# Kernel optimization log

Measured on AMD Instinct MI355X. Metric: run time of the kernel, lower is better.

## Reference

```python
import jax, jax.numpy as jnp
import numpy as np

B, T, H, NUM_LAYERS = 256, 1024, 128, 2


def _lstm_layer(x, W_ih, W_hh, b_ih, b_hh):
    """Single LSTM layer, PyTorch gate order (i, f, g, o).
    x: [B, T, in], W_ih: [4H, in], W_hh: [4H, H], biases: [4H]. Returns [B, T, H].
    """
    Bv = x.shape[0]
    Hv = W_hh.shape[1]
    # Precompute input-to-gate projections for all timesteps (big GEMM outside scan)
    xg = jnp.einsum('bti,gi->btg', x, W_ih) + b_ih + b_hh  # [B, T, 4H]

    def step(carry, xg_t):
        h, c = carry
        g = xg_t + h @ W_hh.T  # [B, 4H]
        i, f, gg, o = jnp.split(g, 4, axis=-1)
        i = jax.nn.sigmoid(i)
        f = jax.nn.sigmoid(f)
        gg = jnp.tanh(gg)
        o = jax.nn.sigmoid(o)
        c = f * c + i * gg
        h = o * jnp.tanh(c)
        return (h, c), h

    h0 = jnp.zeros((Bv, Hv), x.dtype)
    c0 = jnp.zeros((Bv, Hv), x.dtype)
    _, hs = jax.lax.scan(step, (h0, c0), jnp.swapaxes(xg, 0, 1))  # hs: [T, B, H]
    return jnp.swapaxes(hs, 0, 1)


def setup_inputs() -> dict:
    key = jax.random.key(0)
    ks = jax.random.split(key, 11)
    s = 1.0 / np.sqrt(H)  # PyTorch LSTM init scale
    inp = {
        'x': jax.random.normal(ks[0], (B, T, 1), dtype=jnp.float32),
        'W_ih0': jax.random.uniform(ks[1], (4 * H, 1), minval=-s, maxval=s, dtype=jnp.float32),
        'W_hh0': jax.random.uniform(ks[2], (4 * H, H), minval=-s, maxval=s, dtype=jnp.float32),
        'b_ih0': jax.random.uniform(ks[3], (4 * H,), minval=-s, maxval=s, dtype=jnp.float32),
        'b_hh0': jax.random.uniform(ks[4], (4 * H,), minval=-s, maxval=s, dtype=jnp.float32),
        'W_ih1': jax.random.uniform(ks[5], (4 * H, H), minval=-s, maxval=s, dtype=jnp.float32),
        'W_hh1': jax.random.uniform(ks[6], (4 * H, H), minval=-s, maxval=s, dtype=jnp.float32),
        'b_ih1': jax.random.uniform(ks[7], (4 * H,), minval=-s, maxval=s, dtype=jnp.float32),
        'b_hh1': jax.random.uniform(ks[8], (4 * H,), minval=-s, maxval=s, dtype=jnp.float32),
        'fc_w': jax.random.uniform(ks[9], (1, H), minval=-s, maxval=s, dtype=jnp.float32),
        'fc_b': jax.random.uniform(ks[10], (1,), minval=-s, maxval=s, dtype=jnp.float32),
    }
    return inp


def reference(x, W_ih0, W_hh0, b_ih0, b_hh0, W_ih1, W_hh1, b_ih1, b_hh1, fc_w, fc_b):
    h = _lstm_layer(x, W_ih0, W_hh0, b_ih0, b_hh0)   # [B, T, H]
    h = _lstm_layer(h, W_ih1, W_hh1, b_ih1, b_hh1)   # [B, T, H]
    out = jnp.einsum('bth,oh->bto', h, fc_w) + fc_b  # [B, T, 1]
    return out
```

## Files before the change

kernel.cpp:

```cpp
#include <hip/hip_runtime.h>

#define TT 1024
#define HH 128

typedef unsigned int u32;
typedef unsigned short u16;
typedef _Float16 f16;
typedef f16 f16x2 __attribute__((ext_vector_type(2)));
typedef f16 f16x8 __attribute__((ext_vector_type(8)));
typedef float f32x4 __attribute__((ext_vector_type(4)));
typedef u32 u32x4 __attribute__((ext_vector_type(4)));

#define MFMA16(A, B, C) __builtin_amdgcn_mfma_f32_16x16x32_f16((A), (B), (C), 0, 0, 0)
#define K2L2E 2.8853900817779268f

__device__ __forceinline__ float ex2(float x) {
#if __has_builtin(__builtin_amdgcn_exp2f)
    return __builtin_amdgcn_exp2f(x);
#else
    extern "C" __device__ float __ocml_exp2_f32(float);
    return __ocml_exp2_f32(x);
#endif
}
__device__ __forceinline__ float rcp_(float x) { return __builtin_amdgcn_rcpf(x); }

__device__ __forceinline__ float fdot2_(u32 w, u32 h, float acc) {
#if __has_builtin(__builtin_amdgcn_fdot2)
    return __builtin_amdgcn_fdot2(__builtin_bit_cast(f16x2, w),
                                  __builtin_bit_cast(f16x2, h), acc, false);
#else
    const f16x2 a = __builtin_bit_cast(f16x2, w);
    const f16x2 b = __builtin_bit_cast(f16x2, h);
    return fmaf((float)a.y, (float)b.y, fmaf((float)a.x, (float)b.x, acc));
#endif
}

__device__ __forceinline__ float dpp_mov(float v, const int ctrl) {
    int t;
    switch (ctrl) {
      case 0x00: t = __builtin_amdgcn_update_dpp(0, __float_as_int(v), 0x00, 0xF, 0xF, true); break;
      case 0x55: t = __builtin_amdgcn_update_dpp(0, __float_as_int(v), 0x55, 0xF, 0xF, true); break;
      case 0xAA: t = __builtin_amdgcn_update_dpp(0, __float_as_int(v), 0xAA, 0xF, 0xF, true); break;
      case 0xFF: t = __builtin_amdgcn_update_dpp(0, __float_as_int(v), 0xFF, 0xF, 0xF, true); break;
      case 0xB1: t = __builtin_amdgcn_update_dpp(0, __float_as_int(v), 0xB1, 0xF, 0xF, true); break;
      default:   t = __builtin_amdgcn_update_dpp(0, __float_as_int(v), 0x4E, 0xF, 0xF, true); break;
    }
    return __int_as_float(t);
}
__device__ __forceinline__ float dpp_add(float v, const int ctrl) {
    int t;
    switch (ctrl) {
      case 0xB1:  t = __builtin_amdgcn_update_dpp(0, __float_as_int(v), 0xB1,  0xF, 0xF, true); break;
      case 0x4E:  t = __builtin_amdgcn_update_dpp(0, __float_as_int(v), 0x4E,  0xF, 0xF, true); break;
      case 0x141: t = __builtin_amdgcn_update_dpp(0, __float_as_int(v), 0x141, 0xF, 0xF, true); break;
      default:    t = __builtin_amdgcn_update_dpp(0, __float_as_int(v), 0x140, 0xF, 0xF, true); break;
    }
    return v + __int_as_float(t);
}

__device__ __forceinline__ int hswz(int iu) {
    return (iu & 0x30) + (((((iu >> 2) & 3) + (iu >> 4)) & 3) << 2) + (iu & 3);
}

__device__ __forceinline__ float xpose4(float a0, float a1, float a2, float a3, int q) {
    const bool qb0 = (q & 1) != 0;
    float s0, s1;
    {
        const float send = qb0 ? a0 : a1;
        s0 = (qb0 ? a1 : a0) + dpp_mov(send, 0xB1);
    }
    {
        const float send = qb0 ? a2 : a3;
        s1 = (qb0 ? a3 : a2) + dpp_mov(send, 0xB1);
    }
    const bool qb1 = (q & 2) != 0;
    const float send = qb1 ? s0 : s1;
    return (qb1 ? s1 : s0) + dpp_mov(send, 0x4E);
}

__global__ void prep(const float* __restrict__ Whh0, const float* __restrict__ Whh1,
                     const float* __restrict__ Wih1, const float* __restrict__ Wih0,
                     const float* __restrict__ bih0, const float* __restrict__ bhh0,
                     const float* __restrict__ bih1, const float* __restrict__ bhh1,
                     f16* __restrict__ Wpk0, f16* __restrict__ Wpk1,
                     f16* __restrict__ W1h,  f16* __restrict__ W1l,
                     float* __restrict__ bx0, float* __restrict__ wx0,
                     float* __restrict__ b1p)
{
    const int p = blockIdx.x;
    const int k = threadIdx.x;
    const int c = p & 3, u = p >> 2;
    const int g = c * 128 + u;
    const float sc = (c == 2) ? K2L2E : -1.4426950408889634f;

    Wpk0[p * HH + k] = (f16)(Whh0[(size_t)g * HH + k] * sc);
    Wpk1[p * HH + k] = (f16)(Whh1[(size_t)g * HH + k] * sc);
    const float wf = Wih1[(size_t)g * HH + k] * sc;
    const f16 wh = (f16)wf;
    W1h[p * HH + k] = wh;
    W1l[p * HH + k] = (f16)(wf - (float)wh);
    if (k == 0) {
        bx0[p] = (bih0[g] + bhh0[g]) * sc;
        wx0[p] = Wih0[g] * sc;
        b1p[p] = (bih1[g] + bhh1[g]) * sc;
    }
}

__global__ __launch_bounds__(512, 2) void lstm0(
    const float* __restrict__ x, const f16* __restrict__ Wpk0,
    const float* __restrict__ bx0, const float* __restrict__ wx0,
    f16* __restrict__ h0g)
{
    const int b = blockIdx.x;
    const int tid = threadIdx.x;
    const int u = tid >> 2, q = tid & 3;
    const bool is_g = (q == 2);
    const float Ag = is_g ? -2.f : 1.f;
    const float Cg = is_g ?  1.f : 0.f;

    __shared__ __align__(16) float xS[TT];
    __shared__ __align__(16) u32 hS[2][64];
    __shared__ __align__(16) u16 hO[32][HH];

    xS[tid]       = x[(size_t)b * TT + tid];
    xS[tid + 512] = x[(size_t)b * TT + tid + 512];
    if (tid < 128) ((u32*)hS)[tid] = 0u;

    u32x4 Wq[4][4];
#pragma unroll
    for (int c = 0; c < 4; ++c) {
        const u32* wp = (const u32*)Wpk0 + (size_t)((tid & ~3) + c) * 64 + q * 16;
#pragma unroll
        for (int rb = 0; rb < 4; ++rb) Wq[c][rb] = *(const u32x4*)(wp + rb * 4);
    }
    const float biasx = bx0[tid];
    const float wxv   = wx0[tid];
    float c1 = 0.f;
    __syncthreads();

    f16* og = h0g + (size_t)b * TT * HH;

#pragma unroll 1
    for (int t = 0; t < TT; ++t) {
        const u32* hcur = hS[t & 1];
        float a0 = 0.f, a1 = 0.f, a2 = 0.f, a3 = 0.f;
#pragma unroll
        for (int rb = 0; rb < 4; ++rb) {
            const u32x4 hq = *(const u32x4*)(hcur + (q << 4) + (((rb + q) & 3) << 2));
            a0 = fdot2_(Wq[0][rb].x, hq.x, a0); a0 = fdot2_(Wq[0][rb].y, hq.y, a0);
            a0 = fdot2_(Wq[0][rb].z, hq.z, a0); a0 = fdot2_(Wq[0][rb].w, hq.w, a0);
            a1 = fdot2_(Wq[1][rb].x, hq.x, a1); a1 = fdot2_(Wq[1][rb].y, hq.y, a1);
            a1 = fdot2_(Wq[1][rb].z, hq.z, a1); a1 = fdot2_(Wq[1][rb].w, hq.w, a1);
            a2 = fdot2_(Wq[2][rb].x, hq.x, a2); a2 = fdot2_(Wq[2][rb].y, hq.y, a2);
            a2 = fdot2_(Wq[2][rb].z, hq.z, a2); a2 = fdot2_(Wq[2][rb].w, hq.w, a2);
            a3 = fdot2_(Wq[3][rb].x, hq.x, a3); a3 = fdot2_(Wq[3][rb].y, hq.y, a3);
            a3 = fdot2_(Wq[3][rb].z, hq.z, a3); a3 = fdot2_(Wq[3][rb].w, hq.w, a3);
        }
        const float V = xpose4(a0, a1, a2, a3, q);
        const float a = V + fmaf(xS[t], wxv, biasx);
        const float act = fmaf(Ag, rcp_(1.f + ex2(a)), Cg);
        const float gi = dpp_mov(act, 0x00);
        const float gf = dpp_mov(act, 0x55);
        const float gg = dpp_mov(act, 0xAA);
        const float go = dpp_mov(act, 0xFF);
        c1 = fmaf(gf, c1, gi * gg);
        const float h = go * fmaf(-2.f, rcp_(1.f + ex2(K2L2E * c1)), 1.f);
        if (q == 0) {
            const u16 hb = __builtin_bit_cast(u16, (f16)h);
            ((u16*)hS[(t + 1) & 1])[2 * hswz(u >> 1) + (u & 1)] = hb;
            hO[t & 31][u] = hb;
        }
        __syncthreads();
        if ((t & 31) == 31) {
            *(u32x4*)((u16*)og + (size_t)(t - 31) * HH + tid * 8) =
                *(const u32x4*)(&hO[0][0] + tid * 8);
            __syncthreads();
        }
    }
}

__global__ __launch_bounds__(512, 2) void lstm1(
    const f16* __restrict__ h0g, const f16* __restrict__ Wpk1,
    const f16* __restrict__ W1h, const f16* __restrict__ W1l,
    const float* __restrict__ b1p, const float* __restrict__ fcw,
    const float* __restrict__ fcb, float* __restrict__ out)
{
    const int b = blockIdx.x;
    const int tid = threadIdx.x;
    const int u = tid >> 2, q = tid & 3;
    const int wv = tid >> 6, lane = tid & 63;
    const int lr = lane & 15, lq = lane >> 4;
    const bool is_g = (q == 2);
    const float Ag = is_g ? -2.f : 1.f;
    const float Cg = is_g ?  1.f : 0.f;

    __shared__ __align__(16) float xgS[32 * 512];
    __shared__ __align__(16) u32 hS1[2][64];
    __shared__ __align__(16) float fcP[32][16];

    if (tid < 128) ((u32*)hS1)[tid] = 0u;
    const float fcu025 = fcw[u] * 0.25f;
    const float fcbv = fcb[0];
    float c1 = 0.f;
    __syncthreads();

    const f16* hb0 = h0g + (size_t)b * TT * HH;
    float* ob = out + (size_t)b * TT;

#pragma unroll 1
    for (int t0 = 0; t0 < TT; t0 += 32) {
        {
            f16x8 B0[4], B1[4];
#pragma unroll
            for (int ks = 0; ks < 4; ++ks) {
                B0[ks] = *(const f16x8*)(hb0 + (size_t)(t0 + lr) * HH + ks * 32 + lq * 8);
                B1[ks] = *(const f16x8*)(hb0 + (size_t)(t0 + 16 + lr) * HH + ks * 32 + lq * 8);
            }
#pragma unroll
            for (int gtl = 0; gtl < 4; ++gtl) {
                const int g16 = (wv * 4 + gtl) * 16;
                const float4 bi = *(const float4*)&b1p[g16 + lq * 4];
                f32x4 a0 = {bi.x, bi.y, bi.z, bi.w};
                f32x4 a1 = a0;
#pragma unroll
                for (int ks = 0; ks < 4; ++ks) {
                    const f16x8 Ah = *(const f16x8*)(W1h + (size_t)(g16 + lr) * HH + ks * 32 + lq * 8);
                    const f16x8 Al = *(const f16x8*)(W1l + (size_t)(g16 + lr) * HH + ks * 32 + lq * 8);
                    a0 = MFMA16(Ah, B0[ks], a0);
                    a0 = MFMA16(Al, B0[ks], a0);
                    a1 = MFMA16(Ah, B1[ks], a1);
                    a1 = MFMA16(Al, B1[ks], a1);
                }
                const int gb = g16 + lq * 4;
                *(f32x4*)&xgS[lr * 512 + (gb ^ ((lr & 7) << 2))] = a0;
                *(f32x4*)&xgS[(16 + lr) * 512 + (gb ^ ((lr & 7) << 2))] = a1;
            }
        }
        __syncthreads();

        u32x4 Wq[4][4];
        {
            const u32* wb = (const u32*)Wpk1;
            asm volatile("" : "+v"(wb));
#pragma unroll
            for (int c = 0; c < 4; ++c) {
                const u32* wp = wb + (size_t)((tid & ~3) + c) * 64 + q * 16;
#pragma unroll
                for (int rb = 0; rb < 4; ++rb) Wq[c][rb] = *(const u32x4*)(wp + rb * 4);
            }
        }

#pragma unroll 1
        for (int i = 0; i < 32; ++i) {
            const int t = t0 + i;
            const u32* hcur = hS1[t & 1];
            float a0 = 0.f, a1 = 0.f, a2 = 0.f, a3 = 0.f;
#pragma unroll
            for (int rb = 0; rb < 4; ++rb) {
                const u32x4 hq = *(const u32x4*)(hcur + (q << 4) + (((rb + q) & 3) << 2));
                a0 = fdot2_(Wq[0][rb].x, hq.x, a0); a0 = fdot2_(Wq[0][rb].y, hq.y, a0);
                a0 = fdot2_(Wq[0][rb].z, hq.z, a0); a0 = fdot2_(Wq[0][rb].w, hq.w, a0);
                a1 = fdot2_(Wq[1][rb].x, hq.x, a1); a1 = fdot2_(Wq[1][rb].y, hq.y, a1);
                a1 = fdot2_(Wq[1][rb].z, hq.z, a1); a1 = fdot2_(Wq[1][rb].w, hq.w, a1);
                a2 = fdot2_(Wq[2][rb].x, hq.x, a2); a2 = fdot2_(Wq[2][rb].y, hq.y, a2);
                a2 = fdot2_(Wq[2][rb].z, hq.z, a2); a2 = fdot2_(Wq[2][rb].w, hq.w, a2);
                a3 = fdot2_(Wq[3][rb].x, hq.x, a3); a3 = fdot2_(Wq[3][rb].y, hq.y, a3);
                a3 = fdot2_(Wq[3][rb].z, hq.z, a3); a3 = fdot2_(Wq[3][rb].w, hq.w, a3);
            }
            const float V = xpose4(a0, a1, a2, a3, q);
            const float a = V + xgS[i * 512 + (tid ^ ((i & 7) << 2))];
            const float act = fmaf(Ag, rcp_(1.f + ex2(a)), Cg);
            const float gi = dpp_mov(act, 0x00);
            const float gf = dpp_mov(act, 0x55);
            const float gg = dpp_mov(act, 0xAA);
            const float go = dpp_mov(act, 0xFF);
            c1 = fmaf(gf, c1, gi * gg);
            const float h = go * fmaf(-2.f, rcp_(1.f + ex2(K2L2E * c1)), 1.f);
            if (q == 0)
                ((u16*)hS1[(t + 1) & 1])[2 * hswz(u >> 1) + (u & 1)] =
                    __builtin_bit_cast(u16, (f16)h);

            float pf = h * fcu025;
            pf = dpp_add(pf, 0xB1);
            pf = dpp_add(pf, 0x4E);
            pf = dpp_add(pf, 0x141);
            pf = dpp_add(pf, 0x140);
            pf += __int_as_float(__builtin_amdgcn_ds_swizzle(__float_as_int(pf), 0x401F));
            if ((lane & 31) == 0) fcP[i][wv * 2 + (lane >> 5)] = pf;
            __syncthreads();
        }

        if (tid < 32) {
            float s = 0.f;
#pragma unroll
            for (int r = 0; r < 4; ++r) {
                const float4 v = *(const float4*)&fcP[tid][r * 4];
                s += (v.x + v.y) + (v.z + v.w);
            }
            ob[t0 + tid] = s + fcbv;
        }
    }
}

extern "C" void kernel_launch(void* const* d_in, const int* in_sizes, int n_in,
                              void* d_out, int out_size, void* d_ws, size_t ws_size,
                              hipStream_t stream)
{
    const float* x    = (const float*)d_in[0];
    const float* Wih0 = (const float*)d_in[1];
    const float* Whh0 = (const float*)d_in[2];
    const float* bih0 = (const float*)d_in[3];
    const float* bhh0 = (const float*)d_in[4];
    const float* Wih1 = (const float*)d_in[5];
    const float* Whh1 = (const float*)d_in[6];
    const float* bih1 = (const float*)d_in[7];
    const float* bhh1 = (const float*)d_in[8];
    const float* fcw  = (const float*)d_in[9];
    const float* fcb  = (const float*)d_in[10];
    float* out = (float*)d_out;

    f16* h0g  = (f16*)d_ws;
    f16* Wpk0 = h0g + (size_t)256 * TT * HH;
    f16* Wpk1 = Wpk0 + 512 * HH;
    f16* W1h  = Wpk1 + 512 * HH;
    f16* W1l  = W1h + 512 * HH;
    float* bx0 = (float*)(W1l + 512 * HH);
    float* wx0 = bx0 + 512;
    float* b1p = wx0 + 512;

    prep <<<512, 128, 0, stream>>>(Whh0, Whh1, Wih1, Wih0, bih0, bhh0, bih1, bhh1,
                                   Wpk0, Wpk1, W1h, W1l, bx0, wx0, b1p);
    lstm0<<<256, 512, 0, stream>>>(x, Wpk0, bx0, wx0, h0g);
    lstm1<<<256, 512, 0, stream>>>(h0g, Wpk1, W1h, W1l, b1p, fcw, fcb, out);
}
```

Baseline: 1.269 ms.

## Split layer-0 recurrent dot products across 8 lanes with 1024-thread blocks

Layer-0 LSTM now uses 1024 threads per batch row, with each gate row's 128-wide dot product split across 8 lanes instead of 4. Partial sums are combined with an extra ds_swizzle, and the hidden state uses a padded shared-memory layout to avoid bank conflicts. This halves per-thread fdot2 work and register use on the serial critical path, at the cost of a cross-lane reduction and more threads sharing each barrier. Layer 1 also hoists its xg shared-memory load ahead of the dot products so the load latency overlaps with them.

```diff
diff --git a/kernel.cpp b/kernel.cpp
--- a/kernel.cpp
+++ b/kernel.cpp
@@ -10,6 +10,7 @@
 typedef f16 f16x8 __attribute__((ext_vector_type(8)));
 typedef float f32x4 __attribute__((ext_vector_type(4)));
 typedef u32 u32x4 __attribute__((ext_vector_type(4)));
+typedef u32 u32x2 __attribute__((ext_vector_type(2)));
 
 #define MFMA16(A, B, C) __builtin_amdgcn_mfma_f32_16x16x32_f16((A), (B), (C), 0, 0, 0)
 #define K2L2E 2.8853900817779268f
@@ -106,35 +107,36 @@
     }
 }
 
-__global__ __launch_bounds__(512, 2) void lstm0(
+__global__ __launch_bounds__(1024, 4) void lstm0(
     const float* __restrict__ x, const f16* __restrict__ Wpk0,
     const float* __restrict__ bx0, const float* __restrict__ wx0,
     f16* __restrict__ h0g)
 {
     const int b = blockIdx.x;
     const int tid = threadIdx.x;
-    const int u = tid >> 2, q = tid & 3;
+    const int u = tid >> 3, s = tid & 7;
+    const int q = s & 3;
     const bool is_g = (q == 2);
     const float Ag = is_g ? -2.f : 1.f;
     const float Cg = is_g ?  1.f : 0.f;
 
     __shared__ __align__(16) float xS[TT];
-    __shared__ __align__(16) u32 hS[2][64];
+    __shared__ __align__(16) u32 hS[2][96];
     __shared__ __align__(16) u16 hO[32][HH];
 
-    xS[tid]       = x[(size_t)b * TT + tid];
-    xS[tid + 512] = x[(size_t)b * TT + tid + 512];
-    if (tid < 128) ((u32*)hS)[tid] = 0u;
-
-    u32x4 Wq[4][4];
+    xS[tid] = x[(size_t)b * TT + tid];
+    if (tid < 192) ((u32*)hS)[tid] = 0u;
+
+    u32x4 Wq[4][2];
 #pragma unroll
     for (int c = 0; c < 4; ++c) {
-        const u32* wp = (const u32*)Wpk0 + (size_t)((tid & ~3) + c) * 64 + q * 16;
-#pragma unroll
-        for (int rb = 0; rb < 4; ++rb) Wq[c][rb] = *(const u32x4*)(wp + rb * 4);
-    }
-    const float biasx = bx0[tid];
-    const float wxv   = wx0[tid];
+        const u32* wp = (const u32*)Wpk0 + (size_t)(4 * u + c) * 64 + s * 8;
+        Wq[c][0] = *(const u32x4*)wp;
+        Wq[c][1] = *(const u32x4*)(wp + 4);
+    }
+    const int p_lane = 4 * u + q;
+    const float biasx = bx0[p_lane];
+    const float wxv   = wx0[p_lane];
     float c1 = 0.f;
     __syncthreads();
 
@@ -142,11 +144,11 @@
 
 #pragma unroll 1
     for (int t = 0; t < TT; ++t) {
-        const u32* hcur = hS[t & 1];
+        const u32* hcur = hS[t & 1] + s * 12;
         float a0 = 0.f, a1 = 0.f, a2 = 0.f, a3 = 0.f;
 #pragma unroll
-        for (int rb = 0; rb < 4; ++rb) {
-            const u32x4 hq = *(const u32x4*)(hcur + (q << 4) + (((rb + q) & 3) << 2));
+        for (int rb = 0; rb < 2; ++rb) {
+            const u32x4 hq = *(const u32x4*)(hcur + rb * 4);
             a0 = fdot2_(Wq[0][rb].x, hq.x, a0); a0 = fdot2_(Wq[0][rb].y, hq.y, a0);
             a0 = fdot2_(Wq[0][rb].z, hq.z, a0); a0 = fdot2_(Wq[0][rb].w, hq.w, a0);
             a1 = fdot2_(Wq[1][rb].x, hq.x, a1); a1 = fdot2_(Wq[1][rb].y, hq.y, a1);
@@ -156,7 +158,8 @@
             a3 = fdot2_(Wq[3][rb].x, hq.x, a3); a3 = fdot2_(Wq[3][rb].y, hq.y, a3);
             a3 = fdot2_(Wq[3][rb].z, hq.z, a3); a3 = fdot2_(Wq[3][rb].w, hq.w, a3);
         }
-        const float V = xpose4(a0, a1, a2, a3, q);
+        float V = xpose4(a0, a1, a2, a3, q);
+        V += __int_as_float(__builtin_amdgcn_ds_swizzle(__float_as_int(V), 0x101F));
         const float a = V + fmaf(xS[t], wxv, biasx);
         const float act = fmaf(Ag, rcp_(1.f + ex2(a)), Cg);
         const float gi = dpp_mov(act, 0x00);
@@ -165,15 +168,15 @@
         const float go = dpp_mov(act, 0xFF);
         c1 = fmaf(gf, c1, gi * gg);
         const float h = go * fmaf(-2.f, rcp_(1.f + ex2(K2L2E * c1)), 1.f);
-        if (q == 0) {
+        if (s == 0) {
             const u16 hb = __builtin_bit_cast(u16, (f16)h);
-            ((u16*)hS[(t + 1) & 1])[2 * hswz(u >> 1) + (u & 1)] = hb;
+            ((u16*)hS[(t + 1) & 1])[2 * (12 * (u >> 4) + ((u >> 1) & 7)) + (u & 1)] = hb;
             hO[t & 31][u] = hb;
         }
         __syncthreads();
         if ((t & 31) == 31) {
-            *(u32x4*)((u16*)og + (size_t)(t - 31) * HH + tid * 8) =
-                *(const u32x4*)(&hO[0][0] + tid * 8);
+            *(u32x2*)((u16*)og + (size_t)(t - 31) * HH + tid * 4) =
+                *(const u32x2*)(&hO[0][0] + tid * 4);
             __syncthreads();
         }
     }
@@ -253,6 +256,7 @@
 #pragma unroll 1
         for (int i = 0; i < 32; ++i) {
             const int t = t0 + i;
+            const float xgv = xgS[i * 512 + (tid ^ ((i & 7) << 2))];
             const u32* hcur = hS1[t & 1];
             float a0 = 0.f, a1 = 0.f, a2 = 0.f, a3 = 0.f;
 #pragma unroll
@@ -268,7 +272,7 @@
                 a3 = fdot2_(Wq[3][rb].z, hq.z, a3); a3 = fdot2_(Wq[3][rb].w, hq.w, a3);
             }
             const float V = xpose4(a0, a1, a2, a3, q);
-            const float a = V + xgS[i * 512 + (tid ^ ((i & 7) << 2))];
+            const float a = V + xgv;
             const float act = fmaf(Ag, rcp_(1.f + ex2(a)), Cg);
             const float gi = dpp_mov(act, 0x00);
             const float gf = dpp_mov(act, 0x55);
@@ -330,6 +334,6 @@
 
     prep <<<512, 128, 0, stream>>>(Whh0, Whh1, Wih1, Wih0, bih0, bhh0, bih1, bhh1,
                                    Wpk0, Wpk1, W1h, W1l, bx0, wx0, b1p);
-    lstm0<<<256, 512, 0, stream>>>(x, Wpk0, bx0, wx0, h0g);
+    lstm0<<<256, 1024, 0, stream>>>(x, Wpk0, bx0, wx0, h0g);
     lstm1<<<256, 512, 0, stream>>>(h0g, Wpk1, W1h, W1l, b1p, fcw, fcb, out);
 }
```

After: 1.433 ms. 1.13x slower.

## Fuse both LSTM layers into one producer-consumer kernel with flag handoff

Applied to the files above, without the earlier changes.

Merges the layer-0 and layer-1 kernels into a single 512-block launch. The first 256 blocks run layer 0 and publish a per-batch progress flag after each 32-step chunk. The last 256 blocks spin on that flag and then run layer 1, so the two sequential recurrences overlap in time instead of running back to back. It depends on all 512 blocks being co-resident, since launch bounds rise to 4 blocks per CU; if they are not, the spin-wait can deadlock. It also adds a memset and flag polling overhead.

```diff
diff --git a/kernel.cpp b/kernel.cpp
--- a/kernel.cpp
+++ b/kernel.cpp
@@ -106,154 +106,50 @@
     }
 }
 
-__global__ __launch_bounds__(512, 2) void lstm0(
-    const float* __restrict__ x, const f16* __restrict__ Wpk0,
-    const float* __restrict__ bx0, const float* __restrict__ wx0,
-    f16* __restrict__ h0g)
+__global__ __launch_bounds__(512, 4) void lstm_pc(
+    const float* __restrict__ x,
+    const f16* __restrict__ Wpk0, const float* __restrict__ bx0,
+    const float* __restrict__ wx0, f16* __restrict__ h0g,
+    const f16* __restrict__ Wpk1, const f16* __restrict__ W1h,
+    const f16* __restrict__ W1l,  const float* __restrict__ b1p,
+    const float* __restrict__ fcw, const float* __restrict__ fcb,
+    float* __restrict__ out, int* __restrict__ flags)
 {
-    const int b = blockIdx.x;
     const int tid = threadIdx.x;
-    const int u = tid >> 2, q = tid & 3;
-    const bool is_g = (q == 2);
-    const float Ag = is_g ? -2.f : 1.f;
-    const float Cg = is_g ?  1.f : 0.f;
-
-    __shared__ __align__(16) float xS[TT];
-    __shared__ __align__(16) u32 hS[2][64];
-    __shared__ __align__(16) u16 hO[32][HH];
-
-    xS[tid]       = x[(size_t)b * TT + tid];
-    xS[tid + 512] = x[(size_t)b * TT + tid + 512];
-    if (tid < 128) ((u32*)hS)[tid] = 0u;
-
-    u32x4 Wq[4][4];
-#pragma unroll
-    for (int c = 0; c < 4; ++c) {
-        const u32* wp = (const u32*)Wpk0 + (size_t)((tid & ~3) + c) * 64 + q * 16;
-#pragma unroll
-        for (int rb = 0; rb < 4; ++rb) Wq[c][rb] = *(const u32x4*)(wp + rb * 4);
-    }
-    const float biasx = bx0[tid];
-    const float wxv   = wx0[tid];
-    float c1 = 0.f;
-    __syncthreads();
-
-    f16* og = h0g + (size_t)b * TT * HH;
+
+    __shared__ __align__(16) float bigS[32 * 512];
+    __shared__ __align__(16) u32 hSx[2][64];
+    __shared__ __align__(16) u16 hOx[32][HH];
+    __shared__ __align__(16) float fcPx[32][16];
+
+    if (blockIdx.x < 256) {
+        const int b = blockIdx.x;
+        const int u = tid >> 2, q = tid & 3;
+        const bool is_g = (q == 2);
+        const float Ag = is_g ? -2.f : 1.f;
+        const float Cg = is_g ?  1.f : 0.f;
+
+        bigS[tid]       = x[(size_t)b * TT + tid];
+        bigS[tid + 512] = x[(size_t)b * TT + tid + 512];
+        if (tid < 128) ((u32*)hSx)[tid] = 0u;
+
+        u32x4 Wq[4][4];
+#pragma unroll
+        for (int c = 0; c < 4; ++c) {
+            const u32* wp = (const u32*)Wpk0 + (size_t)((tid & ~3) + c) * 64 + q * 16;
+#pragma unroll
+            for (int rb = 0; rb < 4; ++rb) Wq[c][rb] = *(const u32x4*)(wp + rb * 4);
+        }
+        const float biasx = bx0[tid];
+        const float wxv   = wx0[tid];
+        float c1 = 0.f;
+        __syncthreads();
+
+        f16* og = h0g + (size_t)b * TT * HH;
 
 #pragma unroll 1
-    for (int t = 0; t < TT; ++t) {
-        const u32* hcur = hS[t & 1];
-        float a0 = 0.f, a1 = 0.f, a2 = 0.f, a3 = 0.f;
-#pragma unroll
-        for (int rb = 0; rb < 4; ++rb) {
-            const u32x4 hq = *(const u32x4*)(hcur + (q << 4) + (((rb + q) & 3) << 2));
-            a0 = fdot2_(Wq[0][rb].x, hq.x, a0); a0 = fdot2_(Wq[0][rb].y, hq.y, a0);
-            a0 = fdot2_(Wq[0][rb].z, hq.z, a0); a0 = fdot2_(Wq[0][rb].w, hq.w, a0);
-            a1 = fdot2_(Wq[1][rb].x, hq.x, a1); a1 = fdot2_(Wq[1][rb].y, hq.y, a1);
-            a1 = fdot2_(Wq[1][rb].z, hq.z, a1); a1 = fdot2_(Wq[1][rb].w, hq.w, a1);
-            a2 = fdot2_(Wq[2][rb].x, hq.x, a2); a2 = fdot2_(Wq[2][rb].y, hq.y, a2);
-            a2 = fdot2_(Wq[2][rb].z, hq.z, a2); a2 = fdot2_(Wq[2][rb].w, hq.w, a2);
-            a3 = fdot2_(Wq[3][rb].x, hq.x, a3); a3 = fdot2_(Wq[3][rb].y, hq.y, a3);
-            a3 = fdot2_(Wq[3][rb].z, hq.z, a3); a3 = fdot2_(Wq[3][rb].w, hq.w, a3);
-        }
-        const float V = xpose4(a0, a1, a2, a3, q);
-        const float a = V + fmaf(xS[t], wxv, biasx);
-        const float act = fmaf(Ag, rcp_(1.f + ex2(a)), Cg);
-        const float gi = dpp_mov(act, 0x00);
-        const float gf = dpp_mov(act, 0x55);
-        const float gg = dpp_mov(act, 0xAA);
-        const float go = dpp_mov(act, 0xFF);
-        c1 = fmaf(gf, c1, gi * gg);
-        const float h = go * fmaf(-2.f, rcp_(1.f + ex2(K2L2E * c1)), 1.f);
-        if (q == 0) {
-            const u16 hb = __builtin_bit_cast(u16, (f16)h);
-            ((u16*)hS[(t + 1) & 1])[2 * hswz(u >> 1) + (u & 1)] = hb;
-            hO[t & 31][u] = hb;
-        }
-        __syncthreads();
-        if ((t & 31) == 31) {
-            *(u32x4*)((u16*)og + (size_t)(t - 31) * HH + tid * 8) =
-                *(const u32x4*)(&hO[0][0] + tid * 8);
-            __syncthreads();
-        }
-    }
-}
-
-__global__ __launch_bounds__(512, 2) void lstm1(
-    const f16* __restrict__ h0g, const f16* __restrict__ Wpk1,
-    const f16* __restrict__ W1h, const f16* __restrict__ W1l,
-    const float* __restrict__ b1p, const float* __restrict__ fcw,
-    const float* __restrict__ fcb, float* __restrict__ out)
-{
-    const int b = blockIdx.x;
-    const int tid = threadIdx.x;
-    const int u = tid >> 2, q = tid & 3;
-    const int wv = tid >> 6, lane = tid & 63;
-    const int lr = lane & 15, lq = lane >> 4;
-    const bool is_g = (q == 2);
-    const float Ag = is_g ? -2.f : 1.f;
-    const float Cg = is_g ?  1.f : 0.f;
-
-    __shared__ __align__(16) float xgS[32 * 512];
-    __shared__ __align__(16) u32 hS1[2][64];
-    __shared__ __align__(16) float fcP[32][16];
-
-    if (tid < 128) ((u32*)hS1)[tid] = 0u;
-    const float fcu025 = fcw[u] * 0.25f;
-    const float fcbv = fcb[0];
-    float c1 = 0.f;
-    __syncthreads();
-
-    const f16* hb0 = h0g + (size_t)b * TT * HH;
-    float* ob = out + (size_t)b * TT;
-
-#pragma unroll 1
-    for (int t0 = 0; t0 < TT; t0 += 32) {
-        {
-            f16x8 B0[4], B1[4];
-#pragma unroll
-            for (int ks = 0; ks < 4; ++ks) {
-                B0[ks] = *(const f16x8*)(hb0 + (size_t)(t0 + lr) * HH + ks * 32 + lq * 8);
-                B1[ks] = *(const f16x8*)(hb0 + (size_t)(t0 + 16 + lr) * HH + ks * 32 + lq * 8);
-            }
-#pragma unroll
-            for (int gtl = 0; gtl < 4; ++gtl) {
-                const int g16 = (wv * 4 + gtl) * 16;
-                const float4 bi = *(const float4*)&b1p[g16 + lq * 4];
-                f32x4 a0 = {bi.x, bi.y, bi.z, bi.w};
-                f32x4 a1 = a0;
-#pragma unroll
-                for (int ks = 0; ks < 4; ++ks) {
-                    const f16x8 Ah = *(const f16x8*)(W1h + (size_t)(g16 + lr) * HH + ks * 32 + lq * 8);
-                    const f16x8 Al = *(const f16x8*)(W1l + (size_t)(g16 + lr) * HH + ks * 32 + lq * 8);
-                    a0 = MFMA16(Ah, B0[ks], a0);
-                    a0 = MFMA16(Al, B0[ks], a0);
-                    a1 = MFMA16(Ah, B1[ks], a1);
-                    a1 = MFMA16(Al, B1[ks], a1);
-                }
-                const int gb = g16 + lq * 4;
-                *(f32x4*)&xgS[lr * 512 + (gb ^ ((lr & 7) << 2))] = a0;
-                *(f32x4*)&xgS[(16 + lr) * 512 + (gb ^ ((lr & 7) << 2))] = a1;
-            }
-        }
-        __syncthreads();
-
-        u32x4 Wq[4][4];
-        {
-            const u32* wb = (const u32*)Wpk1;
-            asm volatile("" : "+v"(wb));
-#pragma unroll
-            for (int c = 0; c < 4; ++c) {
-                const u32* wp = wb + (size_t)((tid & ~3) + c) * 64 + q * 16;
-#pragma unroll
-                for (int rb = 0; rb < 4; ++rb) Wq[c][rb] = *(const u32x4*)(wp + rb * 4);
-            }
-        }
-
-#pragma unroll 1
-        for (int i = 0; i < 32; ++i) {
-            const int t = t0 + i;
-            const u32* hcur = hS1[t & 1];
+        for (int t = 0; t < TT; ++t) {
+            const u32* hcur = hSx[t & 1];
             float a0 = 0.f, a1 = 0.f, a2 = 0.f, a3 = 0.f;
 #pragma unroll
             for (int rb = 0; rb < 4; ++rb) {
@@ -268,7 +164,7 @@
                 a3 = fdot2_(Wq[3][rb].z, hq.z, a3); a3 = fdot2_(Wq[3][rb].w, hq.w, a3);
             }
             const float V = xpose4(a0, a1, a2, a3, q);
-            const float a = V + xgS[i * 512 + (tid ^ ((i & 7) << 2))];
+            const float a = V + fmaf(bigS[t], wxv, biasx);
             const float act = fmaf(Ag, rcp_(1.f + ex2(a)), Cg);
             const float gi = dpp_mov(act, 0x00);
             const float gf = dpp_mov(act, 0x55);
@@ -276,28 +172,142 @@
             const float go = dpp_mov(act, 0xFF);
             c1 = fmaf(gf, c1, gi * gg);
             const float h = go * fmaf(-2.f, rcp_(1.f + ex2(K2L2E * c1)), 1.f);
-            if (q == 0)
-                ((u16*)hS1[(t + 1) & 1])[2 * hswz(u >> 1) + (u & 1)] =
-                    __builtin_bit_cast(u16, (f16)h);
-
-            float pf = h * fcu025;
-            pf = dpp_add(pf, 0xB1);
-            pf = dpp_add(pf, 0x4E);
-            pf = dpp_add(pf, 0x141);
-            pf = dpp_add(pf, 0x140);
-            pf += __int_as_float(__builtin_amdgcn_ds_swizzle(__float_as_int(pf), 0x401F));
-            if ((lane & 31) == 0) fcP[i][wv * 2 + (lane >> 5)] = pf;
+            if (q == 0) {
+                const u16 hb = __builtin_bit_cast(u16, (f16)h);
+                ((u16*)hSx[(t + 1) & 1])[2 * hswz(u >> 1) + (u & 1)] = hb;
+                hOx[t & 31][u] = hb;
+            }
             __syncthreads();
+            if ((t & 31) == 31) {
+                *(u32x4*)((u16*)og + (size_t)(t - 31) * HH + tid * 8) =
+                    *(const u32x4*)(&hOx[0][0] + tid * 8);
+                __syncthreads();
+                if (tid == 0) {
+                    __threadfence();
+                    __hip_atomic_store(flags + b, (t >> 5) + 1,
+                                       __ATOMIC_RELEASE, __HIP_MEMORY_SCOPE_AGENT);
+                }
+            }
         }
-
-        if (tid < 32) {
-            float s = 0.f;
-#pragma unroll
-            for (int r = 0; r < 4; ++r) {
-                const float4 v = *(const float4*)&fcP[tid][r * 4];
-                s += (v.x + v.y) + (v.z + v.w);
-            }
-            ob[t0 + tid] = s + fcbv;
+    } else {
+        const int b = blockIdx.x - 256;
+        const int u = tid >> 2, q = tid & 3;
+        const int wv = tid >> 6, lane = tid & 63;
+        const int lr = lane & 15, lq = lane >> 4;
+        const bool is_g = (q == 2);
+        const float Ag = is_g ? -2.f : 1.f;
+        const float Cg = is_g ?  1.f : 0.f;
+
+        if (tid < 128) ((u32*)hSx)[tid] = 0u;
+        const float fcu025 = fcw[u] * 0.25f;
+        const float fcbv = fcb[0];
+        float c1 = 0.f;
+        __syncthreads();
+
+        const f16* hb0 = h0g + (size_t)b * TT * HH;
+        float* ob = out + (size_t)b * TT;
+
+#pragma unroll 1
+        for (int t0 = 0; t0 < TT; t0 += 32) {
+            if (tid == 0) {
+                const int need = (t0 >> 5) + 1;
+                while (__hip_atomic_load(flags + b, __ATOMIC_ACQUIRE,
+                                         __HIP_MEMORY_SCOPE_AGENT) < need)
+                    __builtin_amdgcn_s_sleep(32);
+            }
+            __syncthreads();
+
+            {
+                f16x8 B0[4], B1[4];
+#pragma unroll
+                for (int ks = 0; ks < 4; ++ks) {
+                    B0[ks] = *(const f16x8*)(hb0 + (size_t)(t0 + lr) * HH + ks * 32 + lq * 8);
+                    B1[ks] = *(const f16x8*)(hb0 + (size_t)(t0 + 16 + lr) * HH + ks * 32 + lq * 8);
+                }
+#pragma unroll
+                for (int gtl = 0; gtl < 4; ++gtl) {
+                    const int g16 = (wv * 4 + gtl) * 16;
+                    const float4 bi = *(const float4*)&b1p[g16 + lq * 4];
+                    f32x4 a0 = {bi.x, bi.y, bi.z, bi.w};
+                    f32x4 a1 = a0;
+#pragma unroll
+                    for (int ks = 0; ks < 4; ++ks) {
+                        const f16x8 Ah = *(const f16x8*)(W1h + (size_t)(g16 + lr) * HH + ks * 32 + lq * 8);
+                        const f16x8 Al = *(const f16x8*)(W1l + (size_t)(g16 + lr) * HH + ks * 32 + lq * 8);
+                        a0 = MFMA16(Ah, B0[ks], a0);
+                        a0 = MFMA16(Al, B0[ks], a0);
+                        a1 = MFMA16(Ah, B1[ks], a1);
+                        a1 = MFMA16(Al, B1[ks], a1);
+                    }
+                    const int gb = g16 + lq * 4;
+                    *(f32x4*)&bigS[lr * 512 + (gb ^ ((lr & 7) << 2))] = a0;
+                    *(f32x4*)&bigS[(16 + lr) * 512 + (gb ^ ((lr & 7) << 2))] = a1;
+                }
+            }
+            __syncthreads();
+
+            u32x4 Wq[4][4];
+            {
+                const u32* wb = (const u32*)Wpk1;
+                asm volatile("" : "+v"(wb));
+#pragma unroll
+                for (int c = 0; c < 4; ++c) {
+                    const u32* wp = wb + (size_t)((tid & ~3) + c) * 64 + q * 16;
+#pragma unroll
+                    for (int rb = 0; rb < 4; ++rb) Wq[c][rb] = *(const u32x4*)(wp + rb * 4);
+                }
+            }
+
+#pragma unroll 1
+            for (int i = 0; i < 32; ++i) {
+                const int t = t0 + i;
+                const float xgv = bigS[i * 512 + (tid ^ ((i & 7) << 2))];
+                const u32* hcur = hSx[t & 1];
+                float a0 = 0.f, a1 = 0.f, a2 = 0.f, a3 = 0.f;
+#pragma unroll
+                for (int rb = 0; rb < 4; ++rb) {
+                    const u32x4 hq = *(const u32x4*)(hcur + (q << 4) + (((rb + q) & 3) << 2));
+                    a0 = fdot2_(Wq[0][rb].x, hq.x, a0); a0 = fdot2_(Wq[0][rb].y, hq.y, a0);
+                    a0 = fdot2_(Wq[0][rb].z, hq.z, a0); a0 = fdot2_(Wq[0][rb].w, hq.w, a0);
+                    a1 = fdot2_(Wq[1][rb].x, hq.x, a1); a1 = fdot2_(Wq[1][rb].y, hq.y, a1);
+                    a1 = fdot2_(Wq[1][rb].z, hq.z, a1); a1 = fdot2_(Wq[1][rb].w, hq.w, a1);
+                    a2 = fdot2_(Wq[2][rb].x, hq.x, a2); a2 = fdot2_(Wq[2][rb].y, hq.y, a2);
+                    a2 = fdot2_(Wq[2][rb].z, hq.z, a2); a2 = fdot2_(Wq[2][rb].w, hq.w, a2);
+                    a3 = fdot2_(Wq[3][rb].x, hq.x, a3); a3 = fdot2_(Wq[3][rb].y, hq.y, a3);
+                    a3 = fdot2_(Wq[3][rb].z, hq.z, a3); a3 = fdot2_(Wq[3][rb].w, hq.w, a3);
+                }
+                const float V = xpose4(a0, a1, a2, a3, q);
+                const float a = V + xgv;
+                const float act = fmaf(Ag, rcp_(1.f + ex2(a)), Cg);
+                const float gi = dpp_mov(act, 0x00);
+                const float gf = dpp_mov(act, 0x55);
+                const float gg = dpp_mov(act, 0xAA);
+                const float go = dpp_mov(act, 0xFF);
+                c1 = fmaf(gf, c1, gi * gg);
+                const float h = go * fmaf(-2.f, rcp_(1.f + ex2(K2L2E * c1)), 1.f);
+                if (q == 0)
+                    ((u16*)hSx[(t + 1) & 1])[2 * hswz(u >> 1) + (u & 1)] =
+                        __builtin_bit_cast(u16, (f16)h);
+
+                float pf = h * fcu025;
+                pf = dpp_add(pf, 0xB1);
+                pf = dpp_add(pf, 0x4E);
+                pf = dpp_add(pf, 0x141);
+                pf = dpp_add(pf, 0x140);
+                pf += __int_as_float(__builtin_amdgcn_ds_swizzle(__float_as_int(pf), 0x401F));
+                if ((lane & 31) == 0) fcPx[i][wv * 2 + (lane >> 5)] = pf;
+                __syncthreads();
+            }
+
+            if (tid < 32) {
+                float s = 0.f;
+#pragma unroll
+                for (int r = 0; r < 4; ++r) {
+                    const float4 v = *(const float4*)&fcPx[tid][r * 4];
+                    s += (v.x + v.y) + (v.z + v.w);
+                }
+                ob[t0 + tid] = s + fcbv;
+            }
         }
     }
 }
@@ -327,9 +337,11 @@
     float* bx0 = (float*)(W1l + 512 * HH);
     float* wx0 = bx0 + 512;
     float* b1p = wx0 + 512;
-
-    prep <<<512, 128, 0, stream>>>(Whh0, Whh1, Wih1, Wih0, bih0, bhh0, bih1, bhh1,
-                                   Wpk0, Wpk1, W1h, W1l, bx0, wx0, b1p);
-    lstm0<<<256, 512, 0, stream>>>(x, Wpk0, bx0, wx0, h0g);
-    lstm1<<<256, 512, 0, stream>>>(h0g, Wpk1, W1h, W1l, b1p, fcw, fcb, out);
-}
+    int* flags = (int*)(b1p + 512);
+
+    hipMemsetAsync(flags, 0, 256 * sizeof(int), stream);
+    prep<<<512, 128, 0, stream>>>(Whh0, Whh1, Wih1, Wih0, bih0, bhh0, bih1, bhh1,
+                                  Wpk0, Wpk1, W1h, W1l, bx0, wx0, b1p);
+    lstm_pc<<<512, 512, 0, stream>>>(x, Wpk0, bx0, wx0, h0g, Wpk1, W1h, W1l, b1p,
+                                     fcw, fcb, out, flags);
+}
```

After: 1.394 ms. 1.1x slower.

## Split layer-1 recurrent matvec across 8 lanes per unit pair with 3-stage reduction

Applied to the files above, without the earlier changes.

Reorganizes the layer-1 recurrent h·W_hh work so that each group of 8 threads handles two hidden units and each lane covers a 16-wide K slice, instead of 4 lanes per unit each covering a 32-wide slice. The per-step shared-memory read of h drops from four 16-byte loads to two. The result is reduced across the 8 lanes with two DPP steps and a ds_swizzle xor-4. The h buffer is padded to 96 words with a new indexing to avoid bank conflicts, and the xg load is hoisted ahead of the dot products. The cost is an extra cross-lane reduction stage, including a swizzle that goes through the LDS crossbar, on the serial per-step critical path.

```diff
diff --git a/kernel.cpp b/kernel.cpp
--- a/kernel.cpp
+++ b/kernel.cpp
@@ -56,6 +56,9 @@
       default:    t = __builtin_amdgcn_update_dpp(0, __float_as_int(v), 0x140, 0xF, 0xF, true); break;
     }
     return v + __int_as_float(t);
+}
+__device__ __forceinline__ float swz_xor4(float v) {
+    return __int_as_float(__builtin_amdgcn_ds_swizzle(__float_as_int(v), 0x101F));
 }
 
 __device__ __forceinline__ int hswz(int iu) {
@@ -187,7 +190,9 @@
 {
     const int b = blockIdx.x;
     const int tid = threadIdx.x;
-    const int u = tid >> 2, q = tid & 3;
+    const int p = tid >> 3, s = tid & 7;
+    const int q = s & 3, half = s >> 2;
+    const int ul = 2 * p + half;
     const int wv = tid >> 6, lane = tid & 63;
     const int lr = lane & 15, lq = lane >> 4;
     const bool is_g = (q == 2);
@@ -195,11 +200,11 @@
     const float Cg = is_g ?  1.f : 0.f;
 
     __shared__ __align__(16) float xgS[32 * 512];
-    __shared__ __align__(16) u32 hS1[2][64];
+    __shared__ __align__(16) u32 hS1[2][96];
     __shared__ __align__(16) float fcP[32][16];
 
-    if (tid < 128) ((u32*)hS1)[tid] = 0u;
-    const float fcu025 = fcw[u] * 0.25f;
+    if (tid < 192) ((u32*)hS1)[tid] = 0u;
+    const float fcu025 = fcw[ul] * 0.25f;
     const float fcbv = fcb[0];
     float c1 = 0.f;
     __syncthreads();
@@ -238,37 +243,73 @@
         }
         __syncthreads();
 
-        u32x4 Wq[4][4];
+        u32x4 Wq[2][4][2];
         {
             const u32* wb = (const u32*)Wpk1;
             asm volatile("" : "+v"(wb));
 #pragma unroll
-            for (int c = 0; c < 4; ++c) {
-                const u32* wp = wb + (size_t)((tid & ~3) + c) * 64 + q * 16;
-#pragma unroll
-                for (int rb = 0; rb < 4; ++rb) Wq[c][rb] = *(const u32x4*)(wp + rb * 4);
-            }
+            for (int e = 0; e < 2; ++e)
+#pragma unroll
+                for (int c = 0; c < 4; ++c) {
+                    const u32* wp = wb + (size_t)(4 * (2 * p + e) + c) * 64 + s * 8;
+                    Wq[e][c][0] = *(const u32x4*)wp;
+                    Wq[e][c][1] = *(const u32x4*)(wp + 4);
+                }
         }
 
 #pragma unroll 1
         for (int i = 0; i < 32; ++i) {
             const int t = t0 + i;
-            const u32* hcur = hS1[t & 1];
-            float a0 = 0.f, a1 = 0.f, a2 = 0.f, a3 = 0.f;
-#pragma unroll
-            for (int rb = 0; rb < 4; ++rb) {
-                const u32x4 hq = *(const u32x4*)(hcur + (q << 4) + (((rb + q) & 3) << 2));
-                a0 = fdot2_(Wq[0][rb].x, hq.x, a0); a0 = fdot2_(Wq[0][rb].y, hq.y, a0);
-                a0 = fdot2_(Wq[0][rb].z, hq.z, a0); a0 = fdot2_(Wq[0][rb].w, hq.w, a0);
-                a1 = fdot2_(Wq[1][rb].x, hq.x, a1); a1 = fdot2_(Wq[1][rb].y, hq.y, a1);
-                a1 = fdot2_(Wq[1][rb].z, hq.z, a1); a1 = fdot2_(Wq[1][rb].w, hq.w, a1);
-                a2 = fdot2_(Wq[2][rb].x, hq.x, a2); a2 = fdot2_(Wq[2][rb].y, hq.y, a2);
-                a2 = fdot2_(Wq[2][rb].z, hq.z, a2); a2 = fdot2_(Wq[2][rb].w, hq.w, a2);
-                a3 = fdot2_(Wq[3][rb].x, hq.x, a3); a3 = fdot2_(Wq[3][rb].y, hq.y, a3);
-                a3 = fdot2_(Wq[3][rb].z, hq.z, a3); a3 = fdot2_(Wq[3][rb].w, hq.w, a3);
-            }
-            const float V = xpose4(a0, a1, a2, a3, q);
-            const float a = V + xgS[i * 512 + (tid ^ ((i & 7) << 2))];
+            const float xgv = xgS[i * 512 + (tid ^ ((i & 7) << 2))];
+            const u32* hcur = hS1[t & 1] + s * 12;
+            float acc[2][4] = {};
+#pragma unroll
+            for (int rb = 0; rb < 2; ++rb) {
+                const u32x4 hq = *(const u32x4*)(hcur + rb * 4);
+#pragma unroll
+                for (int e = 0; e < 2; ++e) {
+                    acc[e][0] = fdot2_(Wq[e][0][rb].x, hq.x, acc[e][0]);
+                    acc[e][0] = fdot2_(Wq[e][0][rb].y, hq.y, acc[e][0]);
+                    acc[e][0] = fdot2_(Wq[e][0][rb].z, hq.z, acc[e][0]);
+                    acc[e][0] = fdot2_(Wq[e][0][rb].w, hq.w, acc[e][0]);
+                    acc[e][1] = fdot2_(Wq[e][1][rb].x, hq.x, acc[e][1]);
+                    acc[e][1] = fdot2_(Wq[e][1][rb].y, hq.y, acc[e][1]);
+                    acc[e][1] = fdot2_(Wq[e][1][rb].z, hq.z, acc[e][1]);
+                    acc[e][1] = fdot2_(Wq[e][1][rb].w, hq.w, acc[e][1]);
+                    acc[e][2] = fdot2_(Wq[e][2][rb].x, hq.x, acc[e][2]);
+                    acc[e][2] = fdot2_(Wq[e][2][rb].y, hq.y, acc[e][2]);
+                    acc[e][2] = fdot2_(Wq[e][2][rb].z, hq.z, acc[e][2]);
+                    acc[e][2] = fdot2_(Wq[e][2][rb].w, hq.w, acc[e][2]);
+                    acc[e][3] = fdot2_(Wq[e][3][rb].x, hq.x, acc[e][3]);
+                    acc[e][3] = fdot2_(Wq[e][3][rb].y, hq.y, acc[e][3]);
+                    acc[e][3] = fdot2_(Wq[e][3][rb].z, hq.z, acc[e][3]);
+                    acc[e][3] = fdot2_(Wq[e][3][rb].w, hq.w, acc[e][3]);
+                }
+            }
+
+            const bool b0 = (s & 1) != 0;
+            float w4[4];
+#pragma unroll
+            for (int jj = 0; jj < 4; ++jj) {
+                const int e = jj >> 1, ch = (jj & 1) * 2;
+                const float keep = b0 ? acc[e][ch + 1] : acc[e][ch];
+                const float send = b0 ? acc[e][ch]     : acc[e][ch + 1];
+                w4[jj] = keep + dpp_mov(send, 0xB1);
+            }
+            const bool b1 = (s & 2) != 0;
+            float x2[2];
+#pragma unroll
+            for (int kk = 0; kk < 2; ++kk) {
+                const float keep = b1 ? w4[kk * 2 + 1] : w4[kk * 2];
+                const float send = b1 ? w4[kk * 2]     : w4[kk * 2 + 1];
+                x2[kk] = keep + dpp_mov(send, 0x4E);
+            }
+            const bool b2 = half != 0;
+            const float keep3 = b2 ? x2[1] : x2[0];
+            const float send3 = b2 ? x2[0] : x2[1];
+            const float V = keep3 + swz_xor4(send3);
+
+            const float a = V + xgv;
             const float act = fmaf(Ag, rcp_(1.f + ex2(a)), Cg);
             const float gi = dpp_mov(act, 0x00);
             const float gf = dpp_mov(act, 0x55);
@@ -276,9 +317,10 @@
             const float go = dpp_mov(act, 0xFF);
             c1 = fmaf(gf, c1, gi * gg);
             const float h = go * fmaf(-2.f, rcp_(1.f + ex2(K2L2E * c1)), 1.f);
-            if (q == 0)
-                ((u16*)hS1[(t + 1) & 1])[2 * hswz(u >> 1) + (u & 1)] =
+            if (q == 0) {
+                ((u16*)hS1[(t + 1) & 1])[2 * (12 * (ul >> 4) + ((ul >> 1) & 7)) + (ul & 1)] =
                     __builtin_bit_cast(u16, (f16)h);
+            }
 
             float pf = h * fcu025;
             pf = dpp_add(pf, 0xB1);
@@ -291,13 +333,13 @@
         }
 
         if (tid < 32) {
-            float s = 0.f;
+            float sacc = 0.f;
 #pragma unroll
             for (int r = 0; r < 4; ++r) {
                 const float4 v = *(const float4*)&fcP[tid][r * 4];
-                s += (v.x + v.y) + (v.z + v.w);
-            }
-            ob[t0 + tid] = s + fcbv;
+                sacc += (v.x + v.y) + (v.z + v.w);
+            }
+            ob[t0 + tid] = sacc + fcbv;
         }
     }
 }
```

New measurement: 1.304 ms. 2.7% more time.
